# Kernel tuning notes

Measured on AMD Instinct MI355X. Metric: run time of the kernel, lower is better.

The kernel has to match this reference:

```python
import jax, jax.numpy as jnp
import numpy as np

N_NODES = 40000
N_EDGES = 640000
HIDDEN = 128
HEADS = 8
HEAD_DIM = HIDDEN // HEADS
SCALING = HEAD_DIM ** (-0.5)
EPS = 1e-5


def _linear_params(key, din, dout):
    kw, kb = jax.random.split(key)
    s = 1.0 / np.sqrt(din)
    W = jax.random.uniform(kw, (din, dout), jnp.float32, -s, s)
    b = jax.random.uniform(kb, (dout,), jnp.float32, -s, s)
    return W, b


def setup_inputs() -> dict:
    key = jax.random.key(0)
    ks = jax.random.split(key, 10)
    h = jax.random.normal(ks[0], (N_NODES, HIDDEN), jnp.float32)
    row = jax.random.randint(ks[1], (N_EDGES,), 0, N_NODES)
    col = jax.random.randint(ks[2], (N_EDGES,), 0, N_NODES)
    Wq, bq = _linear_params(ks[3], HIDDEN, HIDDEN)
    Wk, bk = _linear_params(ks[4], HIDDEN, HIDDEN)
    Wv, bv = _linear_params(ks[5], HIDDEN, HIDDEN)
    Wo, bo = _linear_params(ks[6], HIDDEN, HIDDEN)
    W1, bf1 = _linear_params(ks[7], HIDDEN, 2 * HIDDEN)
    W2, bf2 = _linear_params(ks[8], 2 * HIDDEN, HIDDEN)
    g1 = jnp.ones((HIDDEN,), jnp.float32)
    b1 = jnp.zeros((HIDDEN,), jnp.float32)
    g2 = jnp.ones((HIDDEN,), jnp.float32)
    b2 = jnp.zeros((HIDDEN,), jnp.float32)
    return {"h": h, "row": row, "col": col,
            "Wq": Wq, "bq": bq, "Wk": Wk, "bk": bk, "Wv": Wv, "bv": bv,
            "Wo": Wo, "bo": bo, "W1": W1, "bf1": bf1, "W2": W2, "bf2": bf2,
            "g1": g1, "b1": b1, "g2": g2, "b2": b2}


def _batchnorm(x, g, b):
    # training-mode BatchNorm1d over node axis (biased variance)
    mu = jnp.mean(x, axis=0)
    var = jnp.mean((x - mu) ** 2, axis=0)
    return (x - mu) * jax.lax.rsqrt(var + EPS) * g + b


def reference(h, row, col, Wq, bq, Wk, bk, Wv, bv, Wo, bo, W1, bf1, W2, bf2, g1, b1, g2, b2):
    N = h.shape[0]
    # QKV projections, reshaped to (N, head_dim, heads) matching the torch code
    q = ((h @ Wq + bq).reshape(N, HEAD_DIM, HEADS)) * SCALING
    k = (h @ Wk + bk).reshape(N, HEAD_DIM, HEADS)
    v = (h @ Wv + bv).reshape(N, HEAD_DIM, HEADS)
    # bsddmm: per-edge, per-head scores  s[e,h] = sum_d q[row,d,h]*k[col,d,h]
    s = jnp.einsum("edh,edh->eh", q[row], k[col])  # [E, H]
    # sparse softmax over each destination row segment
    m = jax.ops.segment_max(s, row, num_segments=N)  # [N, H]
    e = jnp.exp(s - m[row])
    z = jax.ops.segment_sum(e, row, num_segments=N)  # [N, H]
    attn = e / z[row]  # [E, H]
    # bspmm: out[i,d,h] = sum_{e: row[e]=i} attn[e,h] * v[col[e],d,h]
    out = jax.ops.segment_sum(attn[:, None, :] * v[col], row, num_segments=N)  # [N, Dh, H]
    out = out.reshape(N, HIDDEN) @ Wo + bo
    # residual + BN + GELU
    x = _batchnorm(out + h, g1, b1)
    x = jax.nn.gelu(x, approximate=False)
    # FFN with residual
    y = jax.nn.gelu(x @ W1 + bf1, approximate=False) @ W2 + bf2
    return _batchnorm(x + y, g2, b2)
```

## Files before the change

### kernel.cpp

```cpp
#include <hip/hip_runtime.h>

#define N_NODES 40000
#define N_EDGES 640000
#define HID 128
#define NHEAD 8

typedef __attribute__((ext_vector_type(8))) short short8;
typedef __attribute__((ext_vector_type(4))) short short4v;
typedef __attribute__((ext_vector_type(4))) float f32x4;

static constexpr size_t OFF_QKV  = 0;
static constexpr size_t OFF_AOB  = 30720000;
static constexpr size_t OFF_XB   = 40960000;
static constexpr size_t OFF_TB   = 51200000;
static constexpr size_t OFF_HB   = 71680000;
static constexpr size_t OFF_WQKV = 81920000;
static constexpr size_t OFF_WTO  = 82018304;
static constexpr size_t OFF_WT1  = 82051072;
static constexpr size_t OFF_WT2  = 82116608;
static constexpr size_t OFF_BQKV = 82182144;
static constexpr size_t OFF_DEG  = 82240000;
static constexpr size_t OFF_OFFS = 82400000;
static constexpr size_t OFF_CUR  = 82560000;
static constexpr size_t OFF_COLW = 82720000;
static constexpr size_t OFF_BSUM = 85280000;
static constexpr size_t OFF_ST   = 85281024;

__device__ inline unsigned short f2b(float f) {
    unsigned x = __float_as_uint(f);
    unsigned r = x + 0x7fffu + ((x >> 16) & 1u);
    return (unsigned short)(r >> 16);
}
__device__ inline float b2f(unsigned short u) {
    return __uint_as_float(((unsigned)u) << 16);
}

__global__ void h2b_kernel(const float* __restrict__ h, unsigned short* __restrict__ hb)
{
    const int i = (blockIdx.x * 256 + threadIdx.x) * 8;
    float4 f0 = *(const float4*)(h + i);
    float4 f1 = *(const float4*)(h + i + 4);
    short8 w;
    w[0] = (short)f2b(f0.x); w[1] = (short)f2b(f0.y);
    w[2] = (short)f2b(f0.z); w[3] = (short)f2b(f0.w);
    w[4] = (short)f2b(f1.x); w[5] = (short)f2b(f1.y);
    w[6] = (short)f2b(f1.z); w[7] = (short)f2b(f1.w);
    *(short8*)(hb + i) = w;
}

__global__ void wt_kernel(const float* __restrict__ Wq, const float* __restrict__ Wk,
                          const float* __restrict__ Wv, const float* __restrict__ Wo,
                          const float* __restrict__ W1, const float* __restrict__ W2,
                          const float* __restrict__ bq, const float* __restrict__ bk,
                          const float* __restrict__ bv,
                          unsigned short* __restrict__ WTqkv, unsigned short* __restrict__ WTo,
                          unsigned short* __restrict__ WT1, unsigned short* __restrict__ WT2,
                          float* __restrict__ bqkv)
{
    int i = blockIdx.x * 256 + threadIdx.x;
    if (i < 16384) {
        int k = i >> 7, n = i & 127;
        WTqkv[n * 128 + k] = f2b(0.25f * Wq[i]);
    } else if (i < 32768) {
        int j = i - 16384; int k = j >> 7, n = j & 127;
        WTqkv[(128 + n) * 128 + k] = f2b(Wk[j]);
    } else if (i < 49152) {
        int j = i - 32768; int k = j >> 7, n = j & 127;
        WTqkv[(256 + n) * 128 + k] = f2b(Wv[j]);
    } else if (i < 65536) {
        int j = i - 49152; int k = j >> 7, n = j & 127;
        WTo[n * 128 + k] = f2b(Wo[j]);
    } else if (i < 98304) {
        int j = i - 65536; int k = j >> 8, n = j & 255;
        WT1[n * 128 + k] = f2b(W1[j]);
    } else {
        int j = i - 98304; int k = j >> 7, n = j & 127;
        WT2[n * 256 + k] = f2b(W2[j]);
    }
    if (blockIdx.x == 0 && threadIdx.x < 384) {
        int c = threadIdx.x;
        float v = (c < 128) ? 0.25f * bq[c] : (c < 256) ? bk[c - 128] : bv[c - 256];
        bqkv[c] = v;
    }
}

template<typename TC, typename TR, int K, int NTOT, bool ACT, bool STATS>
__global__ __launch_bounds__(256) void mm_kernel(
    const unsigned short* __restrict__ A, const unsigned short* __restrict__ WT,
    const float* __restrict__ bias, const TR* __restrict__ res,
    TC* __restrict__ C, float* __restrict__ st)
{
    __shared__ unsigned short As[64][136];
    __shared__ unsigned short Bs[128][136];
    const int t = threadIdx.x;
    const int lane = t & 63, wave = t >> 6;
    const int row0 = blockIdx.x * 64;
    const int colOff = blockIdx.y * 128;

    f32x4 acc[4][2];
#pragma unroll
    for (int i = 0; i < 4; ++i)
#pragma unroll
        for (int j = 0; j < 2; ++j) acc[i][j] = (f32x4){0.f, 0.f, 0.f, 0.f};

    for (int k0 = 0; k0 < K; k0 += 128) {
        {
            const int r = t >> 2, kc = (t & 3) * 32;
            const unsigned short* ap = A + (size_t)(row0 + r) * K + k0 + kc;
#pragma unroll
            for (int i = 0; i < 4; ++i)
                *(short8*)&As[r][kc + 8 * i] = *(const short8*)(ap + 8 * i);
        }
        {
            const int n = t >> 1, kc = (t & 1) * 64;
            const unsigned short* wp = WT + (size_t)(colOff + n) * K + k0 + kc;
#pragma unroll
            for (int i = 0; i < 8; ++i)
                *(short8*)&Bs[n][kc + 8 * i] = *(const short8*)(wp + 8 * i);
        }
        __syncthreads();

#pragma unroll
        for (int ks = 0; ks < 4; ++ks) {
            const int kf = ks * 32 + (lane >> 4) * 8;
            short8 af[4], bf_[2];
#pragma unroll
            for (int mi = 0; mi < 4; ++mi)
                af[mi] = *(short8*)&As[mi * 16 + (lane & 15)][kf];
#pragma unroll
            for (int ni = 0; ni < 2; ++ni)
                bf_[ni] = *(short8*)&Bs[wave * 32 + ni * 16 + (lane & 15)][kf];
#pragma unroll
            for (int mi = 0; mi < 4; ++mi)
#pragma unroll
                for (int ni = 0; ni < 2; ++ni)
                    acc[mi][ni] = __builtin_amdgcn_mfma_f32_16x16x32_bf16(
                        af[mi], bf_[ni], acc[mi][ni], 0, 0, 0);
        }
        __syncthreads();
    }

    float csum[2] = {0.f, 0.f}, csq[2] = {0.f, 0.f};
#pragma unroll
    for (int mi = 0; mi < 4; ++mi) {
#pragma unroll
        for (int ni = 0; ni < 2; ++ni) {
            const int c = colOff + wave * 32 + ni * 16 + (lane & 15);
            const float bv_ = bias[c];
#pragma unroll
            for (int reg = 0; reg < 4; ++reg) {
                const int r = row0 + mi * 16 + (lane >> 4) * 4 + reg;
                float val = acc[mi][ni][reg] + bv_;
                if constexpr (!__is_same(TR, void)) {
                    if constexpr (sizeof(TR) == 4)
                        val += ((const float*)res)[(size_t)r * 128 + c];
                    else
                        val += b2f(((const unsigned short*)res)[(size_t)r * 128 + c]);
                }
                if constexpr (ACT)
                    val = 0.5f * val * (1.0f + erff(val * 0.70710678118654752f));
                if constexpr (STATS) {
                    csum[ni] += val;
                    csq[ni]  += val * val;
                }
                if constexpr (sizeof(TC) == 4)
                    ((float*)C)[(size_t)r * NTOT + c] = val;
                else
                    ((unsigned short*)C)[(size_t)r * NTOT + c] = f2b(val);
            }
        }
    }

    if constexpr (STATS) {
#pragma unroll
        for (int ni = 0; ni < 2; ++ni) {
            float s = csum[ni], qq = csq[ni];
            s  += __shfl_xor(s, 16, 64);  s  += __shfl_xor(s, 32, 64);
            qq += __shfl_xor(qq, 16, 64); qq += __shfl_xor(qq, 32, 64);
            if (lane < 16) {
                const int c = wave * 32 + ni * 16 + lane;
                atomicAdd(st + c, s);
                atomicAdd(st + 128 + c, qq);
            }
        }
    }
}

__global__ void count_kernel(const int* __restrict__ row, int* __restrict__ deg)
{
    int e = blockIdx.x * 256 + threadIdx.x;
    if (e < N_EDGES) atomicAdd(deg + row[e], 1);
}

__global__ __launch_bounds__(256) void bsum_kernel(const int* __restrict__ deg,
                                                   int* __restrict__ bsum)
{
    __shared__ int ws[4];
    int idx = blockIdx.x * 256 + threadIdx.x;
    int v = (idx < N_NODES) ? deg[idx] : 0;
#pragma unroll
    for (int ofs = 1; ofs < 64; ofs <<= 1) v += __shfl_xor(v, ofs, 64);
    if ((threadIdx.x & 63) == 0) ws[threadIdx.x >> 6] = v;
    __syncthreads();
    if (threadIdx.x == 0) bsum[blockIdx.x] = ws[0] + ws[1] + ws[2] + ws[3];
}

__global__ __launch_bounds__(256) void scan2_kernel(const int* __restrict__ deg,
                                                    const int* __restrict__ bsum,
                                                    int* __restrict__ offs,
                                                    int* __restrict__ cur)
{
    __shared__ int wsum[4];
    __shared__ int base_s;
    const int t = threadIdx.x, lane = t & 63, w = t >> 6;

    int p = 0;
    for (int i = t; i < blockIdx.x; i += 256) p += bsum[i];
#pragma unroll
    for (int ofs = 1; ofs < 64; ofs <<= 1) p += __shfl_xor(p, ofs, 64);
    if (lane == 0) wsum[w] = p;
    __syncthreads();
    if (t == 0) base_s = wsum[0] + wsum[1] + wsum[2] + wsum[3];
    __syncthreads();

    int idx = blockIdx.x * 256 + t;
    int v = (idx < N_NODES) ? deg[idx] : 0;
    int x = v;
#pragma unroll
    for (int d = 1; d < 64; d <<= 1) {
        int y = __shfl_up(x, d, 64);
        if (lane >= d) x += y;
    }
    __syncthreads();
    if (lane == 63) wsum[w] = x;
    __syncthreads();
    int pre = base_s;
    for (int i = 0; i < w; ++i) pre += wsum[i];
    int excl = pre + x - v;
    if (idx < N_NODES) { offs[idx] = excl; cur[idx] = excl; }
}

__global__ void scatter_kernel(const int* __restrict__ row, const int* __restrict__ col,
                               int* __restrict__ cursor, int* __restrict__ colw)
{
    int e = blockIdx.x * 256 + threadIdx.x;
    if (e < N_EDGES) {
        int pos = atomicAdd(cursor + row[e], 1);
        colw[pos] = col[e];
    }
}

__global__ __launch_bounds__(256) void attn_kernel(
    const unsigned short* __restrict__ qkv, const int* __restrict__ colw,
    const int* __restrict__ offs, const int* __restrict__ deg,
    unsigned short* __restrict__ aob)
{
    const int node = blockIdx.x * 4 + (threadIdx.x >> 6);
    const int lane = threadIdx.x & 63;
    const int c0 = 2 * lane;
    const int start = offs[node];
    const int d = deg[node];

    unsigned qu = *(const unsigned*)(qkv + (size_t)node * 384 + c0);
    float q0 = __uint_as_float(qu << 16);
    float q1 = __uint_as_float(qu & 0xffff0000u);
    float z0 = 0.f, z1 = 0.f, o0 = 0.f, o1 = 0.f;

    for (int base = 0; base < d; base += 64) {
        const int nrem = min(64, d - base);
        int cl = 0;
        if (lane < nrem) cl = colw[start + base + lane];
        int j = 0;
        for (; j + 8 <= nrem; j += 8) {
            unsigned ku[8], vu[8];
#pragma unroll
            for (int u = 0; u < 8; ++u) {
                int cn = __shfl(cl, j + u, 64);
                const unsigned short* rp = qkv + (size_t)cn * 384;
                ku[u] = *(const unsigned*)(rp + 128 + c0);
                vu[u] = *(const unsigned*)(rp + 256 + c0);
            }
#pragma unroll
            for (int u = 0; u < 8; ++u) {
                float p0 = q0 * __uint_as_float(ku[u] << 16);
                float p1 = q1 * __uint_as_float(ku[u] & 0xffff0000u);
#pragma unroll
                for (int ofs = 4; ofs < 64; ofs <<= 1) {
                    p0 += __shfl_xor(p0, ofs, 64);
                    p1 += __shfl_xor(p1, ofs, 64);
                }
                float e0 = __expf(p0), e1 = __expf(p1);
                z0 += e0; z1 += e1;
                o0 = fmaf(e0, __uint_as_float(vu[u] << 16), o0);
                o1 = fmaf(e1, __uint_as_float(vu[u] & 0xffff0000u), o1);
            }
        }
        for (; j < nrem; ++j) {
            int cn = __shfl(cl, j, 64);
            const unsigned short* rp = qkv + (size_t)cn * 384;
            unsigned ku = *(const unsigned*)(rp + 128 + c0);
            unsigned vu = *(const unsigned*)(rp + 256 + c0);
            float p0 = q0 * __uint_as_float(ku << 16);
            float p1 = q1 * __uint_as_float(ku & 0xffff0000u);
#pragma unroll
            for (int ofs = 4; ofs < 64; ofs <<= 1) {
                p0 += __shfl_xor(p0, ofs, 64);
                p1 += __shfl_xor(p1, ofs, 64);
            }
            float e0 = __expf(p0), e1 = __expf(p1);
            z0 += e0; z1 += e1;
            o0 = fmaf(e0, __uint_as_float(vu << 16), o0);
            o1 = fmaf(e1, __uint_as_float(vu & 0xffff0000u), o1);
        }
    }
    float r0 = (d > 0) ? o0 / z0 : 0.f;
    float r1 = (d > 0) ? o1 / z1 : 0.f;
    *(unsigned*)(aob + (size_t)node * HID + c0) =
        (unsigned)f2b(r0) | ((unsigned)f2b(r1) << 16);
}

template<typename TO, bool ACT>
__global__ void bn_kernel(const float* __restrict__ x, const float* __restrict__ st,
                          const float* __restrict__ g, const float* __restrict__ b,
                          TO* __restrict__ out)
{
    const int i = (blockIdx.x * 256 + threadIdx.x) * 4;
    const int c = i & (HID - 1);
    float4 xv = *(const float4*)(x + i);
    float v[4] = {xv.x, xv.y, xv.z, xv.w};
#pragma unroll
    for (int u = 0; u < 4; ++u) {
        const int cc = c + u;
        float mu  = st[cc] * (1.0f / N_NODES);
        float var = st[HID + cc] * (1.0f / N_NODES) - mu * mu;
        float val = (v[u] - mu) * rsqrtf(var + 1e-5f) * g[cc] + b[cc];
        if constexpr (ACT) val = 0.5f * val * (1.0f + erff(val * 0.70710678118654752f));
        v[u] = val;
    }
    if constexpr (sizeof(TO) == 4) {
        *(float4*)((float*)out + i) = (float4){v[0], v[1], v[2], v[3]};
    } else {
        short4v w;
        w[0] = (short)f2b(v[0]); w[1] = (short)f2b(v[1]);
        w[2] = (short)f2b(v[2]); w[3] = (short)f2b(v[3]);
        *(short4v*)((unsigned short*)out + i) = w;
    }
}

extern "C" void kernel_launch(void* const* d_in, const int* in_sizes, int n_in,
                              void* d_out, int out_size, void* d_ws, size_t ws_size,
                              hipStream_t stream)
{
    const float* h   = (const float*)d_in[0];
    const int*   row = (const int*)d_in[1];
    const int*   col = (const int*)d_in[2];
    const float* Wq  = (const float*)d_in[3];
    const float* bq  = (const float*)d_in[4];
    const float* Wk  = (const float*)d_in[5];
    const float* bk  = (const float*)d_in[6];
    const float* Wv  = (const float*)d_in[7];
    const float* bv  = (const float*)d_in[8];
    const float* Wo  = (const float*)d_in[9];
    const float* bo  = (const float*)d_in[10];
    const float* W1  = (const float*)d_in[11];
    const float* bf1 = (const float*)d_in[12];
    const float* W2  = (const float*)d_in[13];
    const float* bf2 = (const float*)d_in[14];
    const float* g1  = (const float*)d_in[15];
    const float* b1  = (const float*)d_in[16];
    const float* g2  = (const float*)d_in[17];
    const float* b2  = (const float*)d_in[18];

    float* out = (float*)d_out;
    char*  ws  = (char*)d_ws;

    unsigned short* qkv  = (unsigned short*)(ws + OFF_QKV);
    unsigned short* aob  = (unsigned short*)(ws + OFF_AOB);
    unsigned short* xb   = (unsigned short*)(ws + OFF_XB);
    unsigned short* tb   = (unsigned short*)(ws + OFF_TB);
    unsigned short* hb   = (unsigned short*)(ws + OFF_HB);
    unsigned short* WTqkv= (unsigned short*)(ws + OFF_WQKV);
    unsigned short* WTo  = (unsigned short*)(ws + OFF_WTO);
    unsigned short* WT1  = (unsigned short*)(ws + OFF_WT1);
    unsigned short* WT2  = (unsigned short*)(ws + OFF_WT2);
    float* bqkv = (float*)(ws + OFF_BQKV);
    int*   deg  = (int*)(ws + OFF_DEG);
    int*   offs = (int*)(ws + OFF_OFFS);
    int*   cur  = (int*)(ws + OFF_CUR);
    int*   colw = (int*)(ws + OFF_COLW);
    int*   bsum = (int*)(ws + OFF_BSUM);
    float* st1  = (float*)(ws + OFF_ST);
    float* st2  = st1 + 256;

    hipMemsetAsync(ws + OFF_DEG, 0, (size_t)N_NODES * 4, stream);
    hipMemsetAsync(ws + OFF_ST,  0, 2048, stream);

    dim3 blk(256);
    const int nScanBlocks = (N_NODES + 255) / 256;

    wt_kernel<<<dim3(512), blk, 0, stream>>>(Wq, Wk, Wv, Wo, W1, W2, bq, bk, bv,
                                             WTqkv, WTo, WT1, WT2, bqkv);
    h2b_kernel<<<dim3(2500), blk, 0, stream>>>(h, hb);

    mm_kernel<unsigned short, void, 128, 384, false, false>
        <<<dim3(625, 3), blk, 0, stream>>>(hb, WTqkv, bqkv, nullptr, qkv, nullptr);

    count_kernel<<<dim3(N_EDGES / 256), blk, 0, stream>>>(row, deg);
    bsum_kernel<<<dim3(nScanBlocks), blk, 0, stream>>>(deg, bsum);
    scan2_kernel<<<dim3(nScanBlocks), blk, 0, stream>>>(deg, bsum, offs, cur);
    scatter_kernel<<<dim3(N_EDGES / 256), blk, 0, stream>>>(row, col, cur, colw);

    attn_kernel<<<dim3(N_NODES / 4), blk, 0, stream>>>(qkv, colw, offs, deg, aob);

    mm_kernel<float, float, 128, 128, false, true>
        <<<dim3(625, 1), blk, 0, stream>>>(aob, WTo, bo, h, out, st1);

    bn_kernel<unsigned short, true>
        <<<dim3(N_NODES * HID / 1024), blk, 0, stream>>>(out, st1, g1, b1, xb);

    mm_kernel<unsigned short, void, 128, 256, true, false>
        <<<dim3(625, 2), blk, 0, stream>>>(xb, WT1, bf1, nullptr, tb, nullptr);

    mm_kernel<float, unsigned short, 256, 128, false, true>
        <<<dim3(625, 1), blk, 0, stream>>>(tb, WT2, bf2, xb, out, st2);

    bn_kernel<float, false>
        <<<dim3(N_NODES * HID / 1024), blk, 0, stream>>>(out, st2, g2, b2, out);
}
```

Before: 259.8 us.

## Enlarge GEMM tiles to 128x128 with 2x2 waves, unroll attention gather deeper

The GEMM kernel now computes a 128x128 output tile per block with a 2x2 wave layout and a K-step of 64. Global loads are issued into registers before the barrier, and the tail row tile is guarded. The scatter kernel stores precomputed row offsets (col*384) so the attention kernel skips a multiply. The attention gather is unrolled 16-wide to keep more loads in flight. The aim is better operand reuse per block and more memory-level parallelism in the gather, at the cost of more registers (lower occupancy) and a partially idle final tile.

```diff
diff --git a/kernel.cpp b/kernel.cpp
--- a/kernel.cpp
+++ b/kernel.cpp
@@ -90,95 +90,106 @@
     const float* __restrict__ bias, const TR* __restrict__ res,
     TC* __restrict__ C, float* __restrict__ st)
 {
-    __shared__ unsigned short As[64][136];
-    __shared__ unsigned short Bs[128][136];
+    __shared__ unsigned short As[128][72];
+    __shared__ unsigned short Bs[128][72];
     const int t = threadIdx.x;
     const int lane = t & 63, wave = t >> 6;
-    const int row0 = blockIdx.x * 64;
+    const int wr = wave >> 1, wc = wave & 1;
+    const int row0 = blockIdx.x * 128;
     const int colOff = blockIdx.y * 128;
 
-    f32x4 acc[4][2];
+    f32x4 acc[4][4];
 #pragma unroll
     for (int i = 0; i < 4; ++i)
 #pragma unroll
-        for (int j = 0; j < 2; ++j) acc[i][j] = (f32x4){0.f, 0.f, 0.f, 0.f};
-
-    for (int k0 = 0; k0 < K; k0 += 128) {
-        {
-            const int r = t >> 2, kc = (t & 3) * 32;
-            const unsigned short* ap = A + (size_t)(row0 + r) * K + k0 + kc;
-#pragma unroll
-            for (int i = 0; i < 4; ++i)
-                *(short8*)&As[r][kc + 8 * i] = *(const short8*)(ap + 8 * i);
-        }
-        {
-            const int n = t >> 1, kc = (t & 1) * 64;
-            const unsigned short* wp = WT + (size_t)(colOff + n) * K + k0 + kc;
-#pragma unroll
-            for (int i = 0; i < 8; ++i)
-                *(short8*)&Bs[n][kc + 8 * i] = *(const short8*)(wp + 8 * i);
-        }
+        for (int j = 0; j < 4; ++j) acc[i][j] = (f32x4){0.f, 0.f, 0.f, 0.f};
+
+    const int r0 = t >> 1;
+    const int ar = min(row0 + r0, N_NODES - 1);
+    const int kc = (t & 1) * 32;
+
+    for (int k0 = 0; k0 < K; k0 += 64) {
+        const unsigned short* ap = A + (size_t)ar * K + k0 + kc;
+        short8 av0 = *(const short8*)(ap);
+        short8 av1 = *(const short8*)(ap + 8);
+        short8 av2 = *(const short8*)(ap + 16);
+        short8 av3 = *(const short8*)(ap + 24);
+        const unsigned short* wp = WT + (size_t)(colOff + r0) * K + k0 + kc;
+        short8 bv0 = *(const short8*)(wp);
+        short8 bv1 = *(const short8*)(wp + 8);
+        short8 bv2 = *(const short8*)(wp + 16);
+        short8 bv3 = *(const short8*)(wp + 24);
         __syncthreads();
-
-#pragma unroll
-        for (int ks = 0; ks < 4; ++ks) {
+        *(short8*)&As[r0][kc]      = av0;
+        *(short8*)&As[r0][kc + 8]  = av1;
+        *(short8*)&As[r0][kc + 16] = av2;
+        *(short8*)&As[r0][kc + 24] = av3;
+        *(short8*)&Bs[r0][kc]      = bv0;
+        *(short8*)&Bs[r0][kc + 8]  = bv1;
+        *(short8*)&Bs[r0][kc + 16] = bv2;
+        *(short8*)&Bs[r0][kc + 24] = bv3;
+        __syncthreads();
+
+#pragma unroll
+        for (int ks = 0; ks < 2; ++ks) {
             const int kf = ks * 32 + (lane >> 4) * 8;
-            short8 af[4], bf_[2];
+            short8 af[4], bf_[4];
 #pragma unroll
             for (int mi = 0; mi < 4; ++mi)
-                af[mi] = *(short8*)&As[mi * 16 + (lane & 15)][kf];
-#pragma unroll
-            for (int ni = 0; ni < 2; ++ni)
-                bf_[ni] = *(short8*)&Bs[wave * 32 + ni * 16 + (lane & 15)][kf];
+                af[mi] = *(short8*)&As[wr * 64 + mi * 16 + (lane & 15)][kf];
+#pragma unroll
+            for (int ni = 0; ni < 4; ++ni)
+                bf_[ni] = *(short8*)&Bs[wc * 64 + ni * 16 + (lane & 15)][kf];
 #pragma unroll
             for (int mi = 0; mi < 4; ++mi)
 #pragma unroll
-                for (int ni = 0; ni < 2; ++ni)
+                for (int ni = 0; ni < 4; ++ni)
                     acc[mi][ni] = __builtin_amdgcn_mfma_f32_16x16x32_bf16(
                         af[mi], bf_[ni], acc[mi][ni], 0, 0, 0);
         }
-        __syncthreads();
-    }
-
-    float csum[2] = {0.f, 0.f}, csq[2] = {0.f, 0.f};
+    }
+
+    float csum[4] = {0.f, 0.f, 0.f, 0.f}, csq[4] = {0.f, 0.f, 0.f, 0.f};
 #pragma unroll
     for (int mi = 0; mi < 4; ++mi) {
 #pragma unroll
-        for (int ni = 0; ni < 2; ++ni) {
-            const int c = colOff + wave * 32 + ni * 16 + (lane & 15);
+        for (int ni = 0; ni < 4; ++ni) {
+            const int c = colOff + wc * 64 + ni * 16 + (lane & 15);
             const float bv_ = bias[c];
 #pragma unroll
             for (int reg = 0; reg < 4; ++reg) {
-                const int r = row0 + mi * 16 + (lane >> 4) * 4 + reg;
-                float val = acc[mi][ni][reg] + bv_;
-                if constexpr (!__is_same(TR, void)) {
-                    if constexpr (sizeof(TR) == 4)
-                        val += ((const float*)res)[(size_t)r * 128 + c];
+                const int r = row0 + wr * 64 + mi * 16 + (lane >> 4) * 4 + reg;
+                if (r < N_NODES) {
+                    float val = acc[mi][ni][reg] + bv_;
+                    if constexpr (!__is_same(TR, void)) {
+                        if constexpr (sizeof(TR) == 4)
+                            val += ((const float*)res)[(size_t)r * 128 + c];
+                        else
+                            val += b2f(((const unsigned short*)res)[(size_t)r * 128 + c]);
+                    }
+                    if constexpr (ACT)
+                        val = 0.5f * val * (1.0f + erff(val * 0.70710678118654752f));
+                    if constexpr (STATS) {
+                        csum[ni] += val;
+                        csq[ni]  += val * val;
+                    }
+                    if constexpr (sizeof(TC) == 4)
+                        ((float*)C)[(size_t)r * NTOT + c] = val;
                     else
-                        val += b2f(((const unsigned short*)res)[(size_t)r * 128 + c]);
+                        ((unsigned short*)C)[(size_t)r * NTOT + c] = f2b(val);
                 }
-                if constexpr (ACT)
-                    val = 0.5f * val * (1.0f + erff(val * 0.70710678118654752f));
-                if constexpr (STATS) {
-                    csum[ni] += val;
-                    csq[ni]  += val * val;
-                }
-                if constexpr (sizeof(TC) == 4)
-                    ((float*)C)[(size_t)r * NTOT + c] = val;
-                else
-                    ((unsigned short*)C)[(size_t)r * NTOT + c] = f2b(val);
             }
         }
     }
 
     if constexpr (STATS) {
 #pragma unroll
-        for (int ni = 0; ni < 2; ++ni) {
+        for (int ni = 0; ni < 4; ++ni) {
             float s = csum[ni], qq = csq[ni];
             s  += __shfl_xor(s, 16, 64);  s  += __shfl_xor(s, 32, 64);
             qq += __shfl_xor(qq, 16, 64); qq += __shfl_xor(qq, 32, 64);
             if (lane < 16) {
-                const int c = wave * 32 + ni * 16 + lane;
+                const int c = wc * 64 + ni * 16 + lane;
                 atomicAdd(st + c, s);
                 atomicAdd(st + 128 + c, qq);
             }
@@ -246,7 +257,7 @@
     int e = blockIdx.x * 256 + threadIdx.x;
     if (e < N_EDGES) {
         int pos = atomicAdd(cursor + row[e], 1);
-        colw[pos] = col[e];
+        colw[pos] = col[e] * 384;
     }
 }
 
@@ -266,51 +277,56 @@
     float q1 = __uint_as_float(qu & 0xffff0000u);
     float z0 = 0.f, z1 = 0.f, o0 = 0.f, o1 = 0.f;
 
+#define ATTN_EDGE(KU, VU)                                              \
+    {                                                                  \
+        float p0 = q0 * __uint_as_float((KU) << 16);                   \
+        float p1 = q1 * __uint_as_float((KU) & 0xffff0000u);           \
+        _Pragma("unroll")                                              \
+        for (int ofs = 4; ofs < 64; ofs <<= 1) {                       \
+            p0 += __shfl_xor(p0, ofs, 64);                             \
+            p1 += __shfl_xor(p1, ofs, 64);                             \
+        }                                                              \
+        float e0 = __expf(p0), e1 = __expf(p1);                        \
+        z0 += e0; z1 += e1;                                            \
+        o0 = fmaf(e0, __uint_as_float((VU) << 16), o0);                \
+        o1 = fmaf(e1, __uint_as_float((VU) & 0xffff0000u), o1);        \
+    }
+
     for (int base = 0; base < d; base += 64) {
         const int nrem = min(64, d - base);
-        int cl = 0;
-        if (lane < nrem) cl = colw[start + base + lane];
+        int cls = 0;
+        if (lane < nrem) cls = colw[start + base + lane];
         int j = 0;
-        for (; j + 8 <= nrem; j += 8) {
-            unsigned ku[8], vu[8];
-#pragma unroll
-            for (int u = 0; u < 8; ++u) {
-                int cn = __shfl(cl, j + u, 64);
-                const unsigned short* rp = qkv + (size_t)cn * 384;
+        for (; j + 16 <= nrem; j += 16) {
+            unsigned ku[16], vu[16];
+#pragma unroll
+            for (int u = 0; u < 16; ++u) {
+                int cs = __shfl(cls, j + u, 64);
+                const unsigned short* rp = qkv + cs;
                 ku[u] = *(const unsigned*)(rp + 128 + c0);
                 vu[u] = *(const unsigned*)(rp + 256 + c0);
             }
 #pragma unroll
+            for (int u = 0; u < 16; ++u) ATTN_EDGE(ku[u], vu[u]);
+        }
+        for (; j + 8 <= nrem; j += 8) {
+            unsigned ku[8], vu[8];
+#pragma unroll
             for (int u = 0; u < 8; ++u) {
-                float p0 = q0 * __uint_as_float(ku[u] << 16);
-                float p1 = q1 * __uint_as_float(ku[u] & 0xffff0000u);
-#pragma unroll
-                for (int ofs = 4; ofs < 64; ofs <<= 1) {
-                    p0 += __shfl_xor(p0, ofs, 64);
-                    p1 += __shfl_xor(p1, ofs, 64);
-                }
-                float e0 = __expf(p0), e1 = __expf(p1);
-                z0 += e0; z1 += e1;
-                o0 = fmaf(e0, __uint_as_float(vu[u] << 16), o0);
-                o1 = fmaf(e1, __uint_as_float(vu[u] & 0xffff0000u), o1);
+                int cs = __shfl(cls, j + u, 64);
+                const unsigned short* rp = qkv + cs;
+                ku[u] = *(const unsigned*)(rp + 128 + c0);
+                vu[u] = *(const unsigned*)(rp + 256 + c0);
             }
+#pragma unroll
+            for (int u = 0; u < 8; ++u) ATTN_EDGE(ku[u], vu[u]);
         }
         for (; j < nrem; ++j) {
-            int cn = __shfl(cl, j, 64);
-            const unsigned short* rp = qkv + (size_t)cn * 384;
+            int cs = __shfl(cls, j, 64);
+            const unsigned short* rp = qkv + cs;
             unsigned ku = *(const unsigned*)(rp + 128 + c0);
             unsigned vu = *(const unsigned*)(rp + 256 + c0);
-            float p0 = q0 * __uint_as_float(ku << 16);
-            float p1 = q1 * __uint_as_float(ku & 0xffff0000u);
-#pragma unroll
-            for (int ofs = 4; ofs < 64; ofs <<= 1) {
-                p0 += __shfl_xor(p0, ofs, 64);
-                p1 += __shfl_xor(p1, ofs, 64);
-            }
-            float e0 = __expf(p0), e1 = __expf(p1);
-            z0 += e0; z1 += e1;
-            o0 = fmaf(e0, __uint_as_float(vu << 16), o0);
-            o1 = fmaf(e1, __uint_as_float(vu & 0xffff0000u), o1);
+            ATTN_EDGE(ku, vu);
         }
     }
     float r0 = (d > 0) ? o0 / z0 : 0.f;
@@ -397,13 +413,14 @@
 
     dim3 blk(256);
     const int nScanBlocks = (N_NODES + 255) / 256;
+    const int nRowTiles   = (N_NODES + 127) / 128;
 
     wt_kernel<<<dim3(512), blk, 0, stream>>>(Wq, Wk, Wv, Wo, W1, W2, bq, bk, bv,
                                              WTqkv, WTo, WT1, WT2, bqkv);
     h2b_kernel<<<dim3(2500), blk, 0, stream>>>(h, hb);
 
     mm_kernel<unsigned short, void, 128, 384, false, false>
-        <<<dim3(625, 3), blk, 0, stream>>>(hb, WTqkv, bqkv, nullptr, qkv, nullptr);
+        <<<dim3(nRowTiles, 3), blk, 0, stream>>>(hb, WTqkv, bqkv, nullptr, qkv, nullptr);
 
     count_kernel<<<dim3(N_EDGES / 256), blk, 0, stream>>>(row, deg);
     bsum_kernel<<<dim3(nScanBlocks), blk, 0, stream>>>(deg, bsum);
@@ -413,16 +430,16 @@
     attn_kernel<<<dim3(N_NODES / 4), blk, 0, stream>>>(qkv, colw, offs, deg, aob);
 
     mm_kernel<float, float, 128, 128, false, true>
-        <<<dim3(625, 1), blk, 0, stream>>>(aob, WTo, bo, h, out, st1);
+        <<<dim3(nRowTiles, 1), blk, 0, stream>>>(aob, WTo, bo, h, out, st1);
 
     bn_kernel<unsigned short, true>
         <<<dim3(N_NODES * HID / 1024), blk, 0, stream>>>(out, st1, g1, b1, xb);
 
     mm_kernel<unsigned short, void, 128, 256, true, false>
-        <<<dim3(625, 2), blk, 0, stream>>>(xb, WT1, bf1, nullptr, tb, nullptr);
+        <<<dim3(nRowTiles, 2), blk, 0, stream>>>(xb, WT1, bf1, nullptr, tb, nullptr);
 
     mm_kernel<float, unsigned short, 256, 128, false, true>
-        <<<dim3(625, 1), blk, 0, stream>>>(tb, WT2, bf2, xb, out, st2);
+        <<<dim3(nRowTiles, 1), blk, 0, stream>>>(tb, WT2, bf2, xb, out, st2);
 
     bn_kernel<float, false>
         <<<dim3(N_NODES * HID / 1024), blk, 0, stream>>>(out, st2, g2, b2, out);
```

New measurement: 306.4 us. 18.0% more time.

## Store K/V in interleaved FP8 and gather one word per lane in attention

Applied to the files above, without the earlier changes.

The QKV projection now writes Q as bf16 into its own buffer and K/V as FP8, interleaved so that each lane's two K and two V values fit in one 32-bit word. The attention gather then does a single 4-byte load per edge per lane instead of two loads from a 384-wide bf16 row, which cuts the random-access traffic that dominates the edge loop. Column indices are pre-scaled in the scatter kernel, and the output-projection residual now reads bf16 h instead of fp32 h. This trades precision in K, V and the residual for less memory traffic, at the risk of larger error against the reference.

```diff
diff --git a/kernel.cpp b/kernel.cpp
--- a/kernel.cpp
+++ b/kernel.cpp
@@ -9,22 +9,23 @@
 typedef __attribute__((ext_vector_type(4))) short short4v;
 typedef __attribute__((ext_vector_type(4))) float f32x4;
 
-static constexpr size_t OFF_QKV  = 0;
-static constexpr size_t OFF_AOB  = 30720000;
-static constexpr size_t OFF_XB   = 40960000;
-static constexpr size_t OFF_TB   = 51200000;
-static constexpr size_t OFF_HB   = 71680000;
-static constexpr size_t OFF_WQKV = 81920000;
-static constexpr size_t OFF_WTO  = 82018304;
-static constexpr size_t OFF_WT1  = 82051072;
-static constexpr size_t OFF_WT2  = 82116608;
-static constexpr size_t OFF_BQKV = 82182144;
-static constexpr size_t OFF_DEG  = 82240000;
-static constexpr size_t OFF_OFFS = 82400000;
-static constexpr size_t OFF_CUR  = 82560000;
-static constexpr size_t OFF_COLW = 82720000;
-static constexpr size_t OFF_BSUM = 85280000;
-static constexpr size_t OFF_ST   = 85281024;
+static constexpr size_t OFF_QB   = 0;
+static constexpr size_t OFF_KV8  = 10240000;
+static constexpr size_t OFF_AOB  = 20480000;
+static constexpr size_t OFF_XB   = 30720000;
+static constexpr size_t OFF_TB   = 40960000;
+static constexpr size_t OFF_HB   = 61440000;
+static constexpr size_t OFF_WQKV = 71680000;
+static constexpr size_t OFF_WTO  = 71778304;
+static constexpr size_t OFF_WT1  = 71811072;
+static constexpr size_t OFF_WT2  = 71876608;
+static constexpr size_t OFF_BQKV = 71942144;
+static constexpr size_t OFF_DEG  = 72000000;
+static constexpr size_t OFF_OFFS = 72160000;
+static constexpr size_t OFF_CUR  = 72320000;
+static constexpr size_t OFF_COLW = 72480000;
+static constexpr size_t OFF_BSUM = 75040000;
+static constexpr size_t OFF_ST   = 75041024;
 
 __device__ inline unsigned short f2b(float f) {
     unsigned x = __float_as_uint(f);
@@ -33,6 +34,9 @@
 }
 __device__ inline float b2f(unsigned short u) {
     return __uint_as_float(((unsigned)u) << 16);
+}
+__device__ inline unsigned char f2fp8(float f) {
+    return (unsigned char)(__builtin_amdgcn_cvt_pk_fp8_f32(f, f, 0, false) & 0xff);
 }
 
 __global__ void h2b_kernel(const float* __restrict__ h, unsigned short* __restrict__ hb)
@@ -84,11 +88,11 @@
     }
 }
 
-template<typename TC, typename TR, int K, int NTOT, bool ACT, bool STATS>
+template<typename TC, typename TR, int K, int NTOT, bool ACT, bool STATS, bool QKVMODE>
 __global__ __launch_bounds__(256) void mm_kernel(
     const unsigned short* __restrict__ A, const unsigned short* __restrict__ WT,
     const float* __restrict__ bias, const TR* __restrict__ res,
-    TC* __restrict__ C, float* __restrict__ st)
+    TC* __restrict__ C, unsigned char* __restrict__ kv8, float* __restrict__ st)
 {
     __shared__ unsigned short As[64][136];
     __shared__ unsigned short Bs[128][136];
@@ -145,7 +149,8 @@
     for (int mi = 0; mi < 4; ++mi) {
 #pragma unroll
         for (int ni = 0; ni < 2; ++ni) {
-            const int c = colOff + wave * 32 + ni * 16 + (lane & 15);
+            const int lc = wave * 32 + ni * 16 + (lane & 15);
+            const int c = colOff + lc;
             const float bv_ = bias[c];
 #pragma unroll
             for (int reg = 0; reg < 4; ++reg) {
@@ -163,10 +168,19 @@
                     csum[ni] += val;
                     csq[ni]  += val * val;
                 }
-                if constexpr (sizeof(TC) == 4)
-                    ((float*)C)[(size_t)r * NTOT + c] = val;
-                else
-                    ((unsigned short*)C)[(size_t)r * NTOT + c] = f2b(val);
+                if constexpr (QKVMODE) {
+                    if (colOff == 0) {
+                        ((unsigned short*)C)[(size_t)r * 128 + lc] = f2b(val);
+                    } else {
+                        const int idx = (lc >> 1) * 4 + (lc & 1) + ((colOff == 256) ? 2 : 0);
+                        kv8[(size_t)r * 256 + idx] = f2fp8(val);
+                    }
+                } else {
+                    if constexpr (sizeof(TC) == 4)
+                        ((float*)C)[(size_t)r * NTOT + c] = val;
+                    else
+                        ((unsigned short*)C)[(size_t)r * NTOT + c] = f2b(val);
+                }
             }
         }
     }
@@ -246,14 +260,14 @@
     int e = blockIdx.x * 256 + threadIdx.x;
     if (e < N_EDGES) {
         int pos = atomicAdd(cursor + row[e], 1);
-        colw[pos] = col[e];
+        colw[pos] = col[e] * 64;
     }
 }
 
 __global__ __launch_bounds__(256) void attn_kernel(
-    const unsigned short* __restrict__ qkv, const int* __restrict__ colw,
-    const int* __restrict__ offs, const int* __restrict__ deg,
-    unsigned short* __restrict__ aob)
+    const unsigned short* __restrict__ qb, const unsigned* __restrict__ kv8,
+    const int* __restrict__ colw, const int* __restrict__ offs,
+    const int* __restrict__ deg, unsigned short* __restrict__ aob)
 {
     const int node = blockIdx.x * 4 + (threadIdx.x >> 6);
     const int lane = threadIdx.x & 63;
@@ -261,56 +275,45 @@
     const int start = offs[node];
     const int d = deg[node];
 
-    unsigned qu = *(const unsigned*)(qkv + (size_t)node * 384 + c0);
+    unsigned qu = *(const unsigned*)(qb + (size_t)node * 128 + c0);
     float q0 = __uint_as_float(qu << 16);
     float q1 = __uint_as_float(qu & 0xffff0000u);
     float z0 = 0.f, z1 = 0.f, o0 = 0.f, o1 = 0.f;
 
+#define ATTN_EDGE_W(W)                                                  \
+    {                                                                   \
+        float p0 = q0 * __builtin_amdgcn_cvt_f32_fp8((int)(W), 0);      \
+        float p1 = q1 * __builtin_amdgcn_cvt_f32_fp8((int)(W), 1);      \
+        _Pragma("unroll")                                               \
+        for (int ofs = 4; ofs < 64; ofs <<= 1) {                        \
+            p0 += __shfl_xor(p0, ofs, 64);                              \
+            p1 += __shfl_xor(p1, ofs, 64);                              \
+        }                                                               \
+        float e0 = __expf(p0), e1 = __expf(p1);                         \
+        z0 += e0; z1 += e1;                                             \
+        o0 = fmaf(e0, __builtin_amdgcn_cvt_f32_fp8((int)(W), 2), o0);   \
+        o1 = fmaf(e1, __builtin_amdgcn_cvt_f32_fp8((int)(W), 3), o1);   \
+    }
+
     for (int base = 0; base < d; base += 64) {
         const int nrem = min(64, d - base);
-        int cl = 0;
-        if (lane < nrem) cl = colw[start + base + lane];
+        int cls = 0;
+        if (lane < nrem) cls = colw[start + base + lane];
         int j = 0;
         for (; j + 8 <= nrem; j += 8) {
-            unsigned ku[8], vu[8];
+            unsigned w[8];
 #pragma unroll
             for (int u = 0; u < 8; ++u) {
-                int cn = __shfl(cl, j + u, 64);
-                const unsigned short* rp = qkv + (size_t)cn * 384;
-                ku[u] = *(const unsigned*)(rp + 128 + c0);
-                vu[u] = *(const unsigned*)(rp + 256 + c0);
+                int cs = __shfl(cls, j + u, 64);
+                w[u] = kv8[cs + lane];
             }
 #pragma unroll
-            for (int u = 0; u < 8; ++u) {
-                float p0 = q0 * __uint_as_float(ku[u] << 16);
-                float p1 = q1 * __uint_as_float(ku[u] & 0xffff0000u);
-#pragma unroll
-                for (int ofs = 4; ofs < 64; ofs <<= 1) {
-                    p0 += __shfl_xor(p0, ofs, 64);
-                    p1 += __shfl_xor(p1, ofs, 64);
-                }
-                float e0 = __expf(p0), e1 = __expf(p1);
-                z0 += e0; z1 += e1;
-                o0 = fmaf(e0, __uint_as_float(vu[u] << 16), o0);
-                o1 = fmaf(e1, __uint_as_float(vu[u] & 0xffff0000u), o1);
-            }
+            for (int u = 0; u < 8; ++u) ATTN_EDGE_W(w[u]);
         }
         for (; j < nrem; ++j) {
-            int cn = __shfl(cl, j, 64);
-            const unsigned short* rp = qkv + (size_t)cn * 384;
-            unsigned ku = *(const unsigned*)(rp + 128 + c0);
-            unsigned vu = *(const unsigned*)(rp + 256 + c0);
-            float p0 = q0 * __uint_as_float(ku << 16);
-            float p1 = q1 * __uint_as_float(ku & 0xffff0000u);
-#pragma unroll
-            for (int ofs = 4; ofs < 64; ofs <<= 1) {
-                p0 += __shfl_xor(p0, ofs, 64);
-                p1 += __shfl_xor(p1, ofs, 64);
-            }
-            float e0 = __expf(p0), e1 = __expf(p1);
-            z0 += e0; z1 += e1;
-            o0 = fmaf(e0, __uint_as_float(vu << 16), o0);
-            o1 = fmaf(e1, __uint_as_float(vu & 0xffff0000u), o1);
+            int cs = __shfl(cls, j, 64);
+            unsigned w = kv8[cs + lane];
+            ATTN_EDGE_W(w);
         }
     }
     float r0 = (d > 0) ? o0 / z0 : 0.f;
@@ -374,7 +377,8 @@
     float* out = (float*)d_out;
     char*  ws  = (char*)d_ws;
 
-    unsigned short* qkv  = (unsigned short*)(ws + OFF_QKV);
+    unsigned short* qb   = (unsigned short*)(ws + OFF_QB);
+    unsigned char*  kv8  = (unsigned char*)(ws + OFF_KV8);
     unsigned short* aob  = (unsigned short*)(ws + OFF_AOB);
     unsigned short* xb   = (unsigned short*)(ws + OFF_XB);
     unsigned short* tb   = (unsigned short*)(ws + OFF_TB);
@@ -402,27 +406,28 @@
                                              WTqkv, WTo, WT1, WT2, bqkv);
     h2b_kernel<<<dim3(2500), blk, 0, stream>>>(h, hb);
 
-    mm_kernel<unsigned short, void, 128, 384, false, false>
-        <<<dim3(625, 3), blk, 0, stream>>>(hb, WTqkv, bqkv, nullptr, qkv, nullptr);
+    mm_kernel<unsigned short, void, 128, 384, false, false, true>
+        <<<dim3(625, 3), blk, 0, stream>>>(hb, WTqkv, bqkv, nullptr, qb, kv8, nullptr);
 
     count_kernel<<<dim3(N_EDGES / 256), blk, 0, stream>>>(row, deg);
     bsum_kernel<<<dim3(nScanBlocks), blk, 0, stream>>>(deg, bsum);
     scan2_kernel<<<dim3(nScanBlocks), blk, 0, stream>>>(deg, bsum, offs, cur);
     scatter_kernel<<<dim3(N_EDGES / 256), blk, 0, stream>>>(row, col, cur, colw);
 
-    attn_kernel<<<dim3(N_NODES / 4), blk, 0, stream>>>(qkv, colw, offs, deg, aob);
-
-    mm_kernel<float, float, 128, 128, false, true>
-        <<<dim3(625, 1), blk, 0, stream>>>(aob, WTo, bo, h, out, st1);
+    attn_kernel<<<dim3(N_NODES / 4), blk, 0, stream>>>(qb, (const unsigned*)kv8,
+                                                       colw, offs, deg, aob);
+
+    mm_kernel<float, unsigned short, 128, 128, false, true, false>
+        <<<dim3(625, 1), blk, 0, stream>>>(aob, WTo, bo, hb, out, nullptr, st1);
 
     bn_kernel<unsigned short, true>
         <<<dim3(N_NODES * HID / 1024), blk, 0, stream>>>(out, st1, g1, b1, xb);
 
-    mm_kernel<unsigned short, void, 128, 256, true, false>
-        <<<dim3(625, 2), blk, 0, stream>>>(xb, WT1, bf1, nullptr, tb, nullptr);
-
-    mm_kernel<float, unsigned short, 256, 128, false, true>
-        <<<dim3(625, 1), blk, 0, stream>>>(tb, WT2, bf2, xb, out, st2);
+    mm_kernel<unsigned short, void, 128, 256, true, false, false>
+        <<<dim3(625, 2), blk, 0, stream>>>(xb, WT1, bf1, nullptr, tb, nullptr, nullptr);
+
+    mm_kernel<float, unsigned short, 256, 128, false, true, false>
+        <<<dim3(625, 1), blk, 0, stream>>>(tb, WT2, bf2, xb, out, nullptr, st2);
 
     bn_kernel<float, false>
         <<<dim3(N_NODES * HID / 1024), blk, 0, stream>>>(out, st2, g2, b2, out);
```

After: 258.3 us. About the same (-0.6%).
